# Performance work log

Hardware: AMD Instinct MI355X
Metric: run time of the kernel (lower is better)

The kernel has to match this reference:

```python
import jax, jax.numpy as jnp
import numpy as np
import math

H = 12  # config['n_heads']

def _ln(x, w, b, eps=1e-5):
    mu = x.mean(-1, keepdims=True)
    var = ((x - mu) ** 2).mean(-1, keepdims=True)
    return (x - mu) / jnp.sqrt(var + eps) * w + b

def setup_inputs() -> dict:
    key = jax.random.key(0)
    B, L, D, R = 2, 1024, 768, 128
    d_head = D // H
    ks = jax.random.split(key, 6)
    s = 0.02
    return {
        "x": jax.random.normal(ks[0], (B, L, D), jnp.float32),
        "Wqkv": jax.random.normal(ks[1], (D, 3 * D), jnp.float32) * s,
        "bqkv": jnp.zeros((3 * D,), jnp.float32),
        "Wb1": jax.random.normal(ks[2], (D, R), jnp.float32) * s,
        "Wb2": jax.random.normal(ks[3], (R, H * 5), jnp.float32) * s,
        "temperature": jnp.ones((1,), jnp.float32) * 0.5,
        "Wproj": jax.random.normal(ks[4], (D, D), jnp.float32) * s,
        "bproj": jnp.zeros((D,), jnp.float32),
        "ln_w": jnp.ones((D,), jnp.float32),
        "ln_b": jnp.zeros((D,), jnp.float32),
        "mn_w": jnp.ones((d_head,), jnp.float32),
        "mn_b": jnp.zeros((d_head,), jnp.float32),
    }

def reference(x, Wqkv, bqkv, Wb1, Wb2, temperature, Wproj, bproj, ln_w, ln_b, mn_w, mn_b):
    B, L, D = x.shape
    d = D // H
    x_norm = _ln(x, ln_w, ln_b)
    qkv = x_norm @ Wqkv + bqkv
    q, k, v = jnp.split(qkv, 3, axis=-1)
    # bottleneck gating operates on raw x (not x_norm), matching the source
    params = (jax.nn.silu(x @ Wb1) @ Wb2).reshape(B, L, H, 5)
    sem_amp = jax.nn.sigmoid(params[..., 0])
    sem_phase = jnp.tanh(params[..., 1]) * math.pi
    ctx_amp = jax.nn.sigmoid(params[..., 2])
    ctx_phase = jnp.tanh(params[..., 3]) * math.pi
    # decay_rate = 0.1 + 0.89*sigmoid(params[...,4]) is computed in the source
    # but never used in the final output path, so it is omitted here.
    temp = jnp.clip(temperature, 0.1, 2.0)  # shape (1,), broadcasts
    interference = jnp.tanh(sem_amp * ctx_amp * jnp.cos(sem_phase - ctx_phase)) * temp
    gate = jax.nn.sigmoid(interference)  # [B,L,H]
    q_f = (jax.nn.elu(q) + 1.0).reshape(B, L, H, d)
    k_f = (jax.nn.elu(k) + 1.0).reshape(B, L, H, d)
    v_f = v.reshape(B, L, H, d)
    # gated KV outer products and causal prefix-sum (linear attention state)
    kv_gated = jnp.einsum('blhd,blhe->blhde', k_f, v_f) * (1.0 + gate)[..., None, None]
    kv_states = jnp.cumsum(kv_gated, axis=1)       # [B,L,H,d,d]
    z_states = jnp.cumsum(k_f, axis=1)             # [B,L,H,d]
    out_num = jnp.einsum('blhd,blhde->blhe', q_f, kv_states)
    den = jnp.sum(q_f * z_states, axis=-1, keepdims=True) + 1e-6
    out = _ln(out_num / den, mn_w, mn_b)           # LayerNorm over d_head
    attn_out = out.reshape(B, L, D)
    return (attn_out @ Wproj + bproj, gate)
```

## Files before the change

### kernel.cpp

```cpp
#include <hip/hip_runtime.h>
#include <hip/hip_bf16.h>
#include <math.h>

constexpr int Bc = 2, Lc = 1024, Dc = 768, Hc = 12, dh = 64, Rc = 128;
constexpr int BL = Bc * Lc;
constexpr int TD = 3 * Dc;
constexpr int CH = 64;
constexpr int NC = Lc / CH;
constexpr int BH = Bc * Hc;

typedef __attribute__((ext_vector_type(8))) short bf16x8;
typedef __attribute__((ext_vector_type(4))) float f32x4;

__device__ __forceinline__ float bf2f(short u) {
    union { float f; unsigned int i; } c;
    c.i = ((unsigned int)(unsigned short)u) << 16;
    return c.f;
}
__device__ __forceinline__ short f2b(float f) {
    __hip_bfloat16 h = __float2bfloat16(f);
    return *reinterpret_cast<short*>(&h);
}

#define GLOAD_LDS16(gp, lp)                                                        \
    __builtin_amdgcn_global_load_lds(                                              \
        (const __attribute__((address_space(1))) void*)(gp),                       \
        (__attribute__((address_space(3))) void*)(lp), 16, 0, 0)

__device__ __forceinline__ void do_transpose(const float* __restrict__ W,
                                             __hip_bfloat16* __restrict__ WT,
                                             int K, int N, int bx, int by,
                                             int tid, float* t) {
    int k0 = by * 32, n0 = bx * 32;
    int r = tid >> 5, c = tid & 31;
#pragma unroll
    for (int i = 0; i < 4; i++)
        t[(r + i * 8) * 33 + c] = W[(size_t)(k0 + r + i * 8) * N + n0 + c];
    __syncthreads();
#pragma unroll
    for (int i = 0; i < 4; i++)
        WT[(size_t)(n0 + r + i * 8) * K + k0 + c] = __float2bfloat16(t[c * 33 + r + i * 8]);
}

constexpr int NT1 = (TD / 32) * (Dc / 32);
constexpr int NT2 = (Dc / 32) * (Dc / 32);
constexpr int NT3 = (Rc / 32) * (Dc / 32);
constexpr int NPREP = NT1 + NT2 + NT3 + BL;

__global__ __launch_bounds__(256)
void prep_kernel(const float* __restrict__ x, const float* __restrict__ ln_w,
                 const float* __restrict__ ln_b,
                 const float* __restrict__ Wqkv, const float* __restrict__ Wproj,
                 const float* __restrict__ Wb1,
                 __hip_bfloat16* __restrict__ xnb, __hip_bfloat16* __restrict__ xb,
                 __hip_bfloat16* __restrict__ WqkvT, __hip_bfloat16* __restrict__ WprojT,
                 __hip_bfloat16* __restrict__ Wb1T) {
    __shared__ float shm[32 * 33];
    int bid = blockIdx.x, tid = threadIdx.x;
    if (bid < NT1) { do_transpose(Wqkv, WqkvT, Dc, TD, bid % 72, bid / 72, tid, shm); return; }
    bid -= NT1;
    if (bid < NT2) { do_transpose(Wproj, WprojT, Dc, Dc, bid % 24, bid / 24, tid, shm); return; }
    bid -= NT2;
    if (bid < NT3) { do_transpose(Wb1, Wb1T, Dc, Rc, bid % 4, bid / 4, tid, shm); return; }
    bid -= NT3;
    int row = bid;
    const float* xr = x + (size_t)row * Dc;
    __hip_bfloat16* yr = xnb + (size_t)row * Dc;
    __hip_bfloat16* xbr = xb + (size_t)row * Dc;
    float v[3];
    float s = 0.f;
#pragma unroll
    for (int i = 0; i < 3; i++) { v[i] = xr[tid + i * 256]; s += v[i]; }
    shm[tid] = s; __syncthreads();
    for (int off = 128; off > 0; off >>= 1) {
        if (tid < off) shm[tid] += shm[tid + off];
        __syncthreads();
    }
    float mu = shm[0] / (float)Dc;
    __syncthreads();
    float s2 = 0.f;
#pragma unroll
    for (int i = 0; i < 3; i++) { float d = v[i] - mu; s2 += d * d; }
    shm[tid] = s2; __syncthreads();
    for (int off = 128; off > 0; off >>= 1) {
        if (tid < off) shm[tid] += shm[tid + off];
        __syncthreads();
    }
    float rstd = rsqrtf(shm[0] / (float)Dc + 1e-5f);
#pragma unroll
    for (int i = 0; i < 3; i++) {
        int c = tid + i * 256;
        yr[c] = __float2bfloat16((v[i] - mu) * rstd * ln_w[c] + ln_b[c]);
        xbr[c] = __float2bfloat16(v[i]);
    }
}

constexpr int NQB = (TD / 128) * (BL / 128);
constexpr int NFAT = NQB + BL / 128;
__global__ __launch_bounds__(512)
void fat_gemm_kernel(const __hip_bfloat16* __restrict__ A1,
                     const __hip_bfloat16* __restrict__ B1,
                     const float* __restrict__ bias1,
                     __hip_bfloat16* __restrict__ C1,
                     const __hip_bfloat16* __restrict__ A2,
                     const __hip_bfloat16* __restrict__ B2,
                     float* __restrict__ C2) {
    __shared__ short lds[2][2][128 * 64];
    int bid = blockIdx.x;
    bid = (bid & 7) * (NFAT / 8) + (bid >> 3);
    bool isq = bid < NQB;
    int bx, by, N;
    const __hip_bfloat16 *A, *BT;
    if (isq) { bx = bid % 18; by = bid / 18; A = A1; BT = B1; N = TD; }
    else     { int b2 = bid - NQB; bx = 0; by = b2; A = A2; BT = B2; N = Rc; }
    const int K = Dc;

    int tid = threadIdx.x;
    int wave = tid >> 6, lane = tid & 63;
    int l16 = lane & 15, l4 = lane >> 4;
    int m0 = by * 128, n0 = bx * 128;

    int ab = wave >> 2;
    int r_in = lane >> 3;
    int s_src = (lane & 7) ^ r_in;
    const __hip_bfloat16* gbase = ab ? (BT + (size_t)n0 * K) : (A + (size_t)m0 * K);
    const __hip_bfloat16* gsrc =
        gbase + (size_t)((wave & 3) * 32 + r_in) * K + s_src * 8;

    int wr = (wave >> 2) * 64, wc = (wave & 3) * 32;
    int xs = l16 & 7;

    f32x4 acc[4][2];
#pragma unroll
    for (int i = 0; i < 4; i++)
#pragma unroll
        for (int j = 0; j < 2; j++) acc[i][j] = f32x4{0.f, 0.f, 0.f, 0.f};

    auto stage = [&](int buf, int kt) {
        const __hip_bfloat16* g = gsrc + kt * 64;
        short* lb = &lds[buf][ab][(wave & 3) * 32 * 64];
#pragma unroll
        for (int i = 0; i < 4; i++)
            GLOAD_LDS16(g + (size_t)i * 8 * K, lb + i * 8 * 64);
    };
    auto compute = [&](int buf) {
        const short* As = &lds[buf][0][0];
        const short* Bs = &lds[buf][1][0];
#pragma unroll
        for (int kk = 0; kk < 2; kk++) {
            bf16x8 af[4], bfr[2];
            int slot = (kk * 4 + l4) ^ xs;
#pragma unroll
            for (int f = 0; f < 4; f++)
                af[f] = *reinterpret_cast<const bf16x8*>(
                    &As[(wr + f * 16 + l16) * 64 + slot * 8]);
#pragma unroll
            for (int f = 0; f < 2; f++)
                bfr[f] = *reinterpret_cast<const bf16x8*>(
                    &Bs[(wc + f * 16 + l16) * 64 + slot * 8]);
#pragma unroll
            for (int i = 0; i < 4; i++)
#pragma unroll
                for (int j = 0; j < 2; j++)
                    acc[i][j] = __builtin_amdgcn_mfma_f32_16x16x32_bf16(
                        af[i], bfr[j], acc[i][j], 0, 0, 0);
        }
    };

    int NT = K / 64;
    int cur = 0;
    stage(0, 0);
    __syncthreads();
    for (int t = 0; t < NT; t++) {
        if (t + 1 < NT) stage(cur ^ 1, t + 1);
        compute(cur);
        if (t + 1 < NT) { __syncthreads(); cur ^= 1; }
    }

    int crow = l4 * 4;
#pragma unroll
    for (int i = 0; i < 4; i++) {
#pragma unroll
        for (int j = 0; j < 2; j++) {
            int col = n0 + wc + j * 16 + l16;
            float bb = isq ? bias1[col] : 0.f;
#pragma unroll
            for (int r = 0; r < 4; r++) {
                int rowm = m0 + wr + i * 16 + crow + r;
                float v = acc[i][j][r] + bb;
                if (isq) {
                    C1[(size_t)rowm * N + col] = __float2bfloat16(v);
                } else {
                    v = v / (1.f + expf(-v));
                    C2[(size_t)rowm * N + col] = v;
                }
            }
        }
    }
}

template <bool OUT_BF16, int ACT>
__global__ __launch_bounds__(512)
void gemm_mfma_kernel(const __hip_bfloat16* __restrict__ A,
                      const __hip_bfloat16* __restrict__ BT,
                      const float* __restrict__ bias,
                      void* __restrict__ Cout, int M, int N, int K, int nbx) {
    __shared__ short lds[2][2][128 * 64];
    int nwg = gridDim.x;
    int bid = blockIdx.x;
    if ((nwg & 7) == 0) bid = (bid & 7) * (nwg >> 3) + (bid >> 3);
    int m0 = (bid / nbx) * 128, n0 = (bid % nbx) * 128;

    int tid = threadIdx.x;
    int wave = tid >> 6, lane = tid & 63;
    int l16 = lane & 15, l4 = lane >> 4;

    int ab = wave >> 2;
    int r_in = lane >> 3;
    int s_src = (lane & 7) ^ r_in;
    const __hip_bfloat16* gbase = ab ? (BT + (size_t)n0 * K) : (A + (size_t)m0 * K);
    const __hip_bfloat16* gsrc =
        gbase + (size_t)((wave & 3) * 32 + r_in) * K + s_src * 8;

    int wr = (wave >> 2) * 64, wc = (wave & 3) * 32;
    int xs = l16 & 7;

    f32x4 acc[4][2];
#pragma unroll
    for (int i = 0; i < 4; i++)
#pragma unroll
        for (int j = 0; j < 2; j++) acc[i][j] = f32x4{0.f, 0.f, 0.f, 0.f};

    auto stage = [&](int buf, int kt) {
        const __hip_bfloat16* g = gsrc + kt * 64;
        short* lb = &lds[buf][ab][(wave & 3) * 32 * 64];
#pragma unroll
        for (int i = 0; i < 4; i++)
            GLOAD_LDS16(g + (size_t)i * 8 * K, lb + i * 8 * 64);
    };
    auto compute = [&](int buf) {
        const short* As = &lds[buf][0][0];
        const short* Bs = &lds[buf][1][0];
#pragma unroll
        for (int kk = 0; kk < 2; kk++) {
            bf16x8 af[4], bfr[2];
            int slot = (kk * 4 + l4) ^ xs;
#pragma unroll
            for (int f = 0; f < 4; f++)
                af[f] = *reinterpret_cast<const bf16x8*>(
                    &As[(wr + f * 16 + l16) * 64 + slot * 8]);
#pragma unroll
            for (int f = 0; f < 2; f++)
                bfr[f] = *reinterpret_cast<const bf16x8*>(
                    &Bs[(wc + f * 16 + l16) * 64 + slot * 8]);
#pragma unroll
            for (int i = 0; i < 4; i++)
#pragma unroll
                for (int j = 0; j < 2; j++)
                    acc[i][j] = __builtin_amdgcn_mfma_f32_16x16x32_bf16(
                        af[i], bfr[j], acc[i][j], 0, 0, 0);
        }
    };

    int NT = K / 64;
    int cur = 0;
    stage(0, 0);
    __syncthreads();
    for (int t = 0; t < NT; t++) {
        if (t + 1 < NT) stage(cur ^ 1, t + 1);
        compute(cur);
        if (t + 1 < NT) { __syncthreads(); cur ^= 1; }
    }

    int crow = l4 * 4;
#pragma unroll
    for (int i = 0; i < 4; i++) {
#pragma unroll
        for (int j = 0; j < 2; j++) {
            int col = n0 + wc + j * 16 + l16;
            float bb = bias ? bias[col] : 0.f;
#pragma unroll
            for (int r = 0; r < 4; r++) {
                int rowm = m0 + wr + i * 16 + crow + r;
                float v = acc[i][j][r] + bb;
                if (ACT == 1) v = v / (1.f + expf(-v));
                if (OUT_BF16)
                    ((__hip_bfloat16*)Cout)[(size_t)rowm * N + col] = __float2bfloat16(v);
                else
                    ((float*)Cout)[(size_t)rowm * N + col] = v;
            }
        }
    }
}

__global__ __launch_bounds__(256)
void phaseA_kernel(const __hip_bfloat16* __restrict__ qkv, const float* __restrict__ tbuf,
                   const float* __restrict__ Wb2, const float* __restrict__ temperature,
                   float* __restrict__ gate_out,
                   float* __restrict__ SU, float* __restrict__ zc) {
    int bid = blockIdx.x;
    int bh = bid >> 4, c = bid & 15;
    int b = bh / Hc, h = bh % Hc;
    int tok0 = b * Lc + c * CH;
    __shared__ float Ks[64 * 64];
    __shared__ float Vs[64 * 64];
    __shared__ float ogs[64];
    int tid = threadIdx.x;
#pragma unroll
    for (int i = 0; i < 2; i++) {
        int c8 = tid + i * 256;
        int tt = c8 >> 3, d8 = (c8 & 7) * 8;
        size_t rowoff = (size_t)(tok0 + tt) * TD + h * dh;
        bf16x8 k8 = *reinterpret_cast<const bf16x8*>(qkv + rowoff + Dc + d8);
        bf16x8 v8 = *reinterpret_cast<const bf16x8*>(qkv + rowoff + 2 * Dc + d8);
        float kf[8], vf[8];
#pragma unroll
        for (int j = 0; j < 8; j++) {
            float kv = bf2f(k8[j]);
            kf[j] = kv > 0.f ? kv + 1.f : expf(kv);
            vf[j] = bf2f(v8[j]);
        }
        *reinterpret_cast<float4*>(&Ks[tt * 64 + d8])     = *reinterpret_cast<float4*>(&kf[0]);
        *reinterpret_cast<float4*>(&Ks[tt * 64 + d8 + 4]) = *reinterpret_cast<float4*>(&kf[4]);
        *reinterpret_cast<float4*>(&Vs[tt * 64 + d8])     = *reinterpret_cast<float4*>(&vf[0]);
        *reinterpret_cast<float4*>(&Vs[tt * 64 + d8 + 4]) = *reinterpret_cast<float4*>(&vf[4]);
    }
    if (tid < 64) {
        const float* tr = tbuf + (size_t)(tok0 + tid) * Rc;
        float p0 = 0.f, p1 = 0.f, p2 = 0.f, p3 = 0.f, p4 = 0.f;
#pragma unroll 4
        for (int r = 0; r < Rc; r++) {
            float tv = tr[r];
            const float* wr = Wb2 + r * (Hc * 5) + h * 5;
            p0 = fmaf(tv, wr[0], p0);
            p1 = fmaf(tv, wr[1], p1);
            p2 = fmaf(tv, wr[2], p2);
            p3 = fmaf(tv, wr[3], p3);
            p4 = fmaf(tv, wr[4], p4);
        }
        const float PI = 3.14159265358979323846f;
        float sem_amp = 1.f / (1.f + expf(-p0));
        float sem_phase = tanhf(p1) * PI;
        float ctx_amp = 1.f / (1.f + expf(-p2));
        float ctx_phase = tanhf(p3) * PI;
        float temp = fminf(fmaxf(temperature[0], 0.1f), 2.0f);
        float inter = tanhf(sem_amp * ctx_amp * cosf(sem_phase - ctx_phase)) * temp;
        float g = 1.f / (1.f + expf(-inter));
        gate_out[(size_t)(tok0 + tid) * Hc + h] = g;
        ogs[tid] = 1.f + g;
    }
    __syncthreads();
    int e = tid & 63, d0 = (tid >> 6) * 16;
    float u[16] = {};
    for (int tt = 0; tt < 64; tt++) {
        float vv = Vs[tt * 64 + e] * ogs[tt];
        float4 k4[4];
#pragma unroll
        for (int q = 0; q < 4; q++)
            k4[q] = *reinterpret_cast<const float4*>(&Ks[tt * 64 + d0 + q * 4]);
        const float* kk = reinterpret_cast<const float*>(k4);
#pragma unroll
        for (int j = 0; j < 16; j++)
            u[j] = fmaf(kk[j], vv, u[j]);
    }
    float* Uo = SU + (size_t)bid * 4096 + e * 64 + d0;
#pragma unroll
    for (int q = 0; q < 4; q++)
        *reinterpret_cast<float4*>(Uo + q * 4) =
            make_float4(u[q * 4], u[q * 4 + 1], u[q * 4 + 2], u[q * 4 + 3]);
    if (tid < 64) {
        float zsum = 0.f;
        for (int tt = 0; tt < 64; tt++) zsum += Ks[tt * 64 + tid];
        zc[bid * 64 + tid] = zsum;
    }
}

__global__ __launch_bounds__(256)
void prefix_kernel(float* __restrict__ SU, float* __restrict__ zc) {
    int gid = blockIdx.x * 256 + threadIdx.x;
    if (gid < BH * 4096) {
        int bh = gid >> 12, i = gid & 4095;
        float* S = SU + (size_t)bh * NC * 4096 + i;
        float r[NC];
#pragma unroll
        for (int cc = 0; cc < NC; cc++) r[cc] = S[cc * 4096];
        float run = 0.f;
#pragma unroll
        for (int cc = 0; cc < NC; cc++) { float tv = r[cc]; S[cc * 4096] = run; run += tv; }
    } else {
        int g2 = gid - BH * 4096;
        if (g2 < BH * 64) {
            int bh = g2 >> 6, i = g2 & 63;
            float* z = zc + (size_t)bh * NC * 64 + i;
            float r[NC];
#pragma unroll
            for (int cc = 0; cc < NC; cc++) r[cc] = z[cc * 64];
            float run = 0.f;
#pragma unroll
            for (int cc = 0; cc < NC; cc++) { float tv = r[cc]; z[cc * 64] = run; run += tv; }
        }
    }
}

constexpr int LQ = 72;
constexpr int LB = 136;
__global__ __launch_bounds__(256)
void phaseC_kernel(const __hip_bfloat16* __restrict__ qkv, const float* __restrict__ gate,
                   const float* __restrict__ SU, const float* __restrict__ zc,
                   const float* __restrict__ mn_w, const float* __restrict__ mn_b,
                   __hip_bfloat16* __restrict__ attn) {
    int bid = blockIdx.x;
    int bh = bid >> 4;
    int b = bh / Hc, h = bh % Hc;
    int tok0 = b * Lc + (bid & 15) * CH;
    __shared__ short Qs[64 * LQ];
    __shared__ short Ks[64 * LQ];
    __shared__ short Ps[64 * LQ];
    __shared__ short Bst[80 * LB];
    int tid = threadIdx.x;
    int wave = tid >> 6, lane = tid & 63;
    int l16 = lane & 15, l4 = lane >> 4;

    const float* SUp = SU + (size_t)bid * 4096;
    const float* zcp = zc + (size_t)bid * 64;

#pragma unroll
    for (int i = 0; i < 2; i++) {
        int c8 = tid + i * 256;
        int tt = c8 >> 3, d8 = (c8 & 7) * 8;
        size_t rowoff = (size_t)(tok0 + tt) * TD + h * dh;
        bf16x8 q8 = *reinterpret_cast<const bf16x8*>(qkv + rowoff + d8);
        bf16x8 k8 = *reinterpret_cast<const bf16x8*>(qkv + rowoff + Dc + d8);
        bf16x8 v8 = *reinterpret_cast<const bf16x8*>(qkv + rowoff + 2 * Dc + d8);
        float gv = 1.f + gate[(size_t)(tok0 + tt) * Hc + h];
        short qo[8], ko[8];
#pragma unroll
        for (int j = 0; j < 8; j++) {
            float qv = bf2f(q8[j]);
            qo[j] = f2b(qv > 0.f ? qv + 1.f : expf(qv));
            float kv = bf2f(k8[j]);
            ko[j] = f2b(kv > 0.f ? kv + 1.f : expf(kv));
            Bst[(d8 + j) * LB + tt] = f2b(bf2f(v8[j]) * gv);
        }
        *reinterpret_cast<bf16x8*>(&Qs[tt * LQ + d8]) = *reinterpret_cast<bf16x8*>(qo);
        *reinterpret_cast<bf16x8*>(&Ks[tt * LQ + d8]) = *reinterpret_cast<bf16x8*>(ko);
        float4 sa = *reinterpret_cast<const float4*>(SUp + tt * 64 + d8);
        float4 sb = *reinterpret_cast<const float4*>(SUp + tt * 64 + d8 + 4);
        short so[8] = { f2b(sa.x), f2b(sa.y), f2b(sa.z), f2b(sa.w),
                        f2b(sb.x), f2b(sb.y), f2b(sb.z), f2b(sb.w) };
        *reinterpret_cast<bf16x8*>(&Bst[tt * LB + 64 + d8]) = *reinterpret_cast<bf16x8*>(so);
    }
    if (tid < 64) {
        Bst[64 * LB + tid] = f2b(1.0f);
        Bst[64 * LB + 64 + tid] = f2b(zcp[tid]);
    } else {
        for (int i2 = tid - 64; i2 < 15 * LB; i2 += 192) Bst[65 * LB + i2] = 0;
    }
    __syncthreads();

    const short* arow = &Qs[(wave * 16 + l16) * LQ];
    f32x4 accp[4];
#pragma unroll
    for (int j = 0; j < 4; j++) accp[j] = f32x4{0.f, 0.f, 0.f, 0.f};
#pragma unroll
    for (int kk = 0; kk < 2; kk++) {
        bf16x8 af = *reinterpret_cast<const bf16x8*>(&arow[kk * 32 + l4 * 8]);
#pragma unroll
        for (int j = 0; j < 4; j++) {
            bf16x8 bfv = *reinterpret_cast<const bf16x8*>(
                &Ks[(j * 16 + l16) * LQ + kk * 32 + l4 * 8]);
            accp[j] = __builtin_amdgcn_mfma_f32_16x16x32_bf16(af, bfv, accp[j], 0, 0, 0);
        }
    }
#pragma unroll
    for (int j = 0; j < 4; j++) {
#pragma unroll
        for (int r = 0; r < 4; r++) {
            int l = wave * 16 + l4 * 4 + r;
            int t = j * 16 + l16;
            float pv = (t <= l) ? accp[j][r] : 0.f;
            Ps[l * LQ + t] = f2b(pv);
        }
    }
    __syncthreads();

    const short* prow = &Ps[(wave * 16 + l16) * LQ];
    f32x4 acc[5];
#pragma unroll
    for (int j = 0; j < 5; j++) acc[j] = f32x4{0.f, 0.f, 0.f, 0.f};
#pragma unroll
    for (int kk = 0; kk < 4; kk++) {
        bf16x8 af = (kk < 2)
            ? *reinterpret_cast<const bf16x8*>(&prow[kk * 32 + l4 * 8])
            : *reinterpret_cast<const bf16x8*>(&arow[(kk - 2) * 32 + l4 * 8]);
#pragma unroll
        for (int j = 0; j < 5; j++) {
            bf16x8 bfv = *reinterpret_cast<const bf16x8*>(
                &Bst[(j * 16 + l16) * LB + kk * 32 + l4 * 8]);
            acc[j] = __builtin_amdgcn_mfma_f32_16x16x32_bf16(af, bfv, acc[j], 0, 0, 0);
        }
    }

#pragma unroll
    for (int r = 0; r < 4; r++) {
        float den = __shfl(acc[4][r], l4 * 16) + 1e-6f;
        float inv = 1.f / den;
        float v0 = acc[0][r] * inv, v1 = acc[1][r] * inv;
        float v2 = acc[2][r] * inv, v3 = acc[3][r] * inv;
        float s1 = v0 + v1 + v2 + v3;
        float s2 = v0 * v0 + v1 * v1 + v2 * v2 + v3 * v3;
#pragma unroll
        for (int m = 1; m < 16; m <<= 1) {
            s1 += __shfl_xor(s1, m, 64);
            s2 += __shfl_xor(s2, m, 64);
        }
        float mu = s1 * (1.f / 64.f);
        float rstd = rsqrtf(s2 * (1.f / 64.f) - mu * mu + 1e-5f);
        int l = wave * 16 + l4 * 4 + r;
        __hip_bfloat16* orow = attn + (size_t)(tok0 + l) * Dc + h * dh;
        float vj[4] = {v0, v1, v2, v3};
#pragma unroll
        for (int j = 0; j < 4; j++) {
            int e = j * 16 + l16;
            orow[e] = __float2bfloat16((vj[j] - mu) * rstd * mn_w[e] + mn_b[e]);
        }
    }
}

extern "C" void kernel_launch(void* const* d_in, const int* in_sizes, int n_in,
                              void* d_out, int out_size, void* d_ws, size_t ws_size,
                              hipStream_t stream) {
    const float* x     = (const float*)d_in[0];
    const float* Wqkv  = (const float*)d_in[1];
    const float* bqkv  = (const float*)d_in[2];
    const float* Wb1   = (const float*)d_in[3];
    const float* Wb2   = (const float*)d_in[4];
    const float* temp  = (const float*)d_in[5];
    const float* Wproj = (const float*)d_in[6];
    const float* bproj = (const float*)d_in[7];
    const float* ln_w  = (const float*)d_in[8];
    const float* ln_b  = (const float*)d_in[9];
    const float* mn_w  = (const float*)d_in[10];
    const float* mn_b  = (const float*)d_in[11];

    float* out0 = (float*)d_out;
    float* gate = out0 + (size_t)BL * Dc;

    float* ws   = (float*)d_ws;
    float* tbuf = ws;
    float* SU   = tbuf + (size_t)BL * Rc;
    float* zc   = SU + (size_t)BH * NC * 4096;
    __hip_bfloat16* bfr = (__hip_bfloat16*)(zc + (size_t)BH * NC * 64);
    __hip_bfloat16* qkvb   = bfr;
    __hip_bfloat16* xnb    = qkvb + (size_t)BL * TD;
    __hip_bfloat16* xb     = xnb + (size_t)BL * Dc;
    __hip_bfloat16* attnb  = xb + (size_t)BL * Dc;
    __hip_bfloat16* WqkvT  = attnb + (size_t)BL * Dc;
    __hip_bfloat16* WprojT = WqkvT + (size_t)TD * Dc;
    __hip_bfloat16* Wb1T   = WprojT + (size_t)Dc * Dc;

    prep_kernel<<<NPREP, 256, 0, stream>>>(x, ln_w, ln_b, Wqkv, Wproj, Wb1,
                                           xnb, xb, WqkvT, WprojT, Wb1T);
    fat_gemm_kernel<<<NFAT, 512, 0, stream>>>(xnb, WqkvT, bqkv, qkvb, xb, Wb1T, tbuf);
    phaseA_kernel<<<BH * NC, 256, 0, stream>>>(qkvb, tbuf, Wb2, temp, gate, SU, zc);
    prefix_kernel<<<(BH * 4096 + BH * 64 + 255) / 256, 256, 0, stream>>>(SU, zc);
    phaseC_kernel<<<BH * NC, 256, 0, stream>>>(qkvb, gate, SU, zc, mn_w, mn_b, attnb);
    gemm_mfma_kernel<false, 0><<<(Dc / 128) * (BL / 128), 512, 0, stream>>>(
        attnb, WprojT, bproj, out0, BL, Dc, Dc, Dc / 128);
}
```

Baseline: 69.94 us.

## Use MFMA for chunk KV state in phaseA and shrink projection GEMM tiles

The per-chunk K^T·(gated V) outer-product sum in phaseA moves from scalar FMAs to bf16 MFMA. K and gated V are stored transposed in LDS, and a ones-row appended to V yields the z column sums from the same MMA. The gate bottleneck dot product is spread over 4 threads per token, with Wb2 staged in LDS and a shuffle reduction. The output projection GEMM switches from 128x128 tiles with 512 threads to 64x64 tiles with 256 threads, giving 384 blocks instead of 96 to fill more CUs. The risk is bf16 rounding of the gated V and K values in the state computation.

```diff
diff --git a/kernel.cpp b/kernel.cpp
--- a/kernel.cpp
+++ b/kernel.cpp
@@ -199,62 +199,59 @@
     }
 }
 
-template <bool OUT_BF16, int ACT>
-__global__ __launch_bounds__(512)
-void gemm_mfma_kernel(const __hip_bfloat16* __restrict__ A,
-                      const __hip_bfloat16* __restrict__ BT,
-                      const float* __restrict__ bias,
-                      void* __restrict__ Cout, int M, int N, int K, int nbx) {
-    __shared__ short lds[2][2][128 * 64];
+__global__ __launch_bounds__(256)
+void gemm64_kernel(const __hip_bfloat16* __restrict__ A,
+                   const __hip_bfloat16* __restrict__ BT,
+                   const float* __restrict__ bias,
+                   float* __restrict__ C, int M, int N, int K, int nbx) {
+    __shared__ short lds[2][128 * 64];
     int nwg = gridDim.x;
     int bid = blockIdx.x;
     if ((nwg & 7) == 0) bid = (bid & 7) * (nwg >> 3) + (bid >> 3);
-    int m0 = (bid / nbx) * 128, n0 = (bid % nbx) * 128;
+    int m0 = (bid / nbx) * 64, n0 = (bid % nbx) * 64;
 
     int tid = threadIdx.x;
     int wave = tid >> 6, lane = tid & 63;
     int l16 = lane & 15, l4 = lane >> 4;
 
-    int ab = wave >> 2;
     int r_in = lane >> 3;
     int s_src = (lane & 7) ^ r_in;
-    const __hip_bfloat16* gbase = ab ? (BT + (size_t)n0 * K) : (A + (size_t)m0 * K);
-    const __hip_bfloat16* gsrc =
-        gbase + (size_t)((wave & 3) * 32 + r_in) * K + s_src * 8;
-
-    int wr = (wave >> 2) * 64, wc = (wave & 3) * 32;
+    const __hip_bfloat16* gsrc = (wave < 2)
+        ? A  + (size_t)(m0 + wave * 32 + r_in) * K + s_src * 8
+        : BT + (size_t)(n0 + (wave - 2) * 32 + r_in) * K + s_src * 8;
+
+    int wr = (wave >> 1) * 32, wc = (wave & 1) * 32;
     int xs = l16 & 7;
 
-    f32x4 acc[4][2];
-#pragma unroll
-    for (int i = 0; i < 4; i++)
+    f32x4 acc[2][2];
+#pragma unroll
+    for (int i = 0; i < 2; i++)
 #pragma unroll
         for (int j = 0; j < 2; j++) acc[i][j] = f32x4{0.f, 0.f, 0.f, 0.f};
 
     auto stage = [&](int buf, int kt) {
         const __hip_bfloat16* g = gsrc + kt * 64;
-        short* lb = &lds[buf][ab][(wave & 3) * 32 * 64];
+        short* lb = &lds[buf][wave * 32 * 64];
 #pragma unroll
         for (int i = 0; i < 4; i++)
             GLOAD_LDS16(g + (size_t)i * 8 * K, lb + i * 8 * 64);
     };
     auto compute = [&](int buf) {
-        const short* As = &lds[buf][0][0];
-        const short* Bs = &lds[buf][1][0];
+        const short* As = &lds[buf][0];
+        const short* Bs = &lds[buf][64 * 64];
 #pragma unroll
         for (int kk = 0; kk < 2; kk++) {
-            bf16x8 af[4], bfr[2];
+            bf16x8 af[2], bfr[2];
             int slot = (kk * 4 + l4) ^ xs;
 #pragma unroll
-            for (int f = 0; f < 4; f++)
-                af[f] = *reinterpret_cast<const bf16x8*>(
+            for (int f = 0; f < 2; f++) {
+                af[f]  = *reinterpret_cast<const bf16x8*>(
                     &As[(wr + f * 16 + l16) * 64 + slot * 8]);
-#pragma unroll
-            for (int f = 0; f < 2; f++)
                 bfr[f] = *reinterpret_cast<const bf16x8*>(
                     &Bs[(wc + f * 16 + l16) * 64 + slot * 8]);
-#pragma unroll
-            for (int i = 0; i < 4; i++)
+            }
+#pragma unroll
+            for (int i = 0; i < 2; i++)
 #pragma unroll
                 for (int j = 0; j < 2; j++)
                     acc[i][j] = __builtin_amdgcn_mfma_f32_16x16x32_bf16(
@@ -274,25 +271,21 @@
 
     int crow = l4 * 4;
 #pragma unroll
-    for (int i = 0; i < 4; i++) {
+    for (int i = 0; i < 2; i++) {
 #pragma unroll
         for (int j = 0; j < 2; j++) {
             int col = n0 + wc + j * 16 + l16;
-            float bb = bias ? bias[col] : 0.f;
+            float bb = bias[col];
 #pragma unroll
             for (int r = 0; r < 4; r++) {
                 int rowm = m0 + wr + i * 16 + crow + r;
-                float v = acc[i][j][r] + bb;
-                if (ACT == 1) v = v / (1.f + expf(-v));
-                if (OUT_BF16)
-                    ((__hip_bfloat16*)Cout)[(size_t)rowm * N + col] = __float2bfloat16(v);
-                else
-                    ((float*)Cout)[(size_t)rowm * N + col] = v;
+                C[(size_t)rowm * N + col] = acc[i][j][r] + bb;
             }
         }
     }
 }
 
+constexpr int LQ = 72;
 __global__ __launch_bounds__(256)
 void phaseA_kernel(const __hip_bfloat16* __restrict__ qkv, const float* __restrict__ tbuf,
                    const float* __restrict__ Wb2, const float* __restrict__ temperature,
@@ -302,76 +295,105 @@
     int bh = bid >> 4, c = bid & 15;
     int b = bh / Hc, h = bh % Hc;
     int tok0 = b * Lc + c * CH;
-    __shared__ float Ks[64 * 64];
-    __shared__ float Vs[64 * 64];
+    __shared__ short KsT[64 * LQ];
+    __shared__ short VT[80 * LQ];
+    __shared__ float w2s[5 * 128];
     __shared__ float ogs[64];
     int tid = threadIdx.x;
+    int wave = tid >> 6, lane = tid & 63;
+    int l16 = lane & 15, l4 = lane >> 4;
+
+    for (int i = tid; i < 640; i += 256) {
+        int cc = i >> 7, r = i & 127;
+        w2s[i] = Wb2[r * (Hc * 5) + h * 5 + cc];
+    }
+    bf16x8 k8[2], v8[2];
 #pragma unroll
     for (int i = 0; i < 2; i++) {
         int c8 = tid + i * 256;
         int tt = c8 >> 3, d8 = (c8 & 7) * 8;
         size_t rowoff = (size_t)(tok0 + tt) * TD + h * dh;
-        bf16x8 k8 = *reinterpret_cast<const bf16x8*>(qkv + rowoff + Dc + d8);
-        bf16x8 v8 = *reinterpret_cast<const bf16x8*>(qkv + rowoff + 2 * Dc + d8);
-        float kf[8], vf[8];
+        k8[i] = *reinterpret_cast<const bf16x8*>(qkv + rowoff + Dc + d8);
+        v8[i] = *reinterpret_cast<const bf16x8*>(qkv + rowoff + 2 * Dc + d8);
+    }
+    for (int i = tid; i < 16 * LQ; i += 256) VT[64 * LQ + i] = 0;
+    if (tid < 64) VT[64 * LQ + tid] = f2b(1.0f);
+    __syncthreads();
+
+    {
+        int tt = tid >> 2, sub = tid & 3;
+        const float* tr = tbuf + (size_t)(tok0 + tt) * Rc + sub * 32;
+        float p[5] = {};
+        for (int r4 = 0; r4 < 32; r4 += 4) {
+            float4 tv = *reinterpret_cast<const float4*>(tr + r4);
+#pragma unroll
+            for (int cc = 0; cc < 5; cc++) {
+                float4 w4 = *reinterpret_cast<const float4*>(&w2s[cc * 128 + sub * 32 + r4]);
+                p[cc] = fmaf(tv.x, w4.x, fmaf(tv.y, w4.y,
+                        fmaf(tv.z, w4.z, fmaf(tv.w, w4.w, p[cc]))));
+            }
+        }
+#pragma unroll
+        for (int cc = 0; cc < 5; cc++) {
+            p[cc] += __shfl_xor(p[cc], 1, 64);
+            p[cc] += __shfl_xor(p[cc], 2, 64);
+        }
+        if (sub == 0) {
+            const float PI = 3.14159265358979323846f;
+            float sem_amp = 1.f / (1.f + expf(-p[0]));
+            float sem_phase = tanhf(p[1]) * PI;
+            float ctx_amp = 1.f / (1.f + expf(-p[2]));
+            float ctx_phase = tanhf(p[3]) * PI;
+            float temp = fminf(fmaxf(temperature[0], 0.1f), 2.0f);
+            float inter = tanhf(sem_amp * ctx_amp * cosf(sem_phase - ctx_phase)) * temp;
+            float g = 1.f / (1.f + expf(-inter));
+            gate_out[(size_t)(tok0 + tt) * Hc + h] = g;
+            ogs[tt] = 1.f + g;
+        }
+    }
+    __syncthreads();
+
+#pragma unroll
+    for (int i = 0; i < 2; i++) {
+        int c8 = tid + i * 256;
+        int tt = c8 >> 3, d8 = (c8 & 7) * 8;
+        float gv = ogs[tt];
 #pragma unroll
         for (int j = 0; j < 8; j++) {
-            float kv = bf2f(k8[j]);
-            kf[j] = kv > 0.f ? kv + 1.f : expf(kv);
-            vf[j] = bf2f(v8[j]);
-        }
-        *reinterpret_cast<float4*>(&Ks[tt * 64 + d8])     = *reinterpret_cast<float4*>(&kf[0]);
-        *reinterpret_cast<float4*>(&Ks[tt * 64 + d8 + 4]) = *reinterpret_cast<float4*>(&kf[4]);
-        *reinterpret_cast<float4*>(&Vs[tt * 64 + d8])     = *reinterpret_cast<float4*>(&vf[0]);
-        *reinterpret_cast<float4*>(&Vs[tt * 64 + d8 + 4]) = *reinterpret_cast<float4*>(&vf[4]);
-    }
-    if (tid < 64) {
-        const float* tr = tbuf + (size_t)(tok0 + tid) * Rc;
-        float p0 = 0.f, p1 = 0.f, p2 = 0.f, p3 = 0.f, p4 = 0.f;
-#pragma unroll 4
-        for (int r = 0; r < Rc; r++) {
-            float tv = tr[r];
-            const float* wr = Wb2 + r * (Hc * 5) + h * 5;
-            p0 = fmaf(tv, wr[0], p0);
-            p1 = fmaf(tv, wr[1], p1);
-            p2 = fmaf(tv, wr[2], p2);
-            p3 = fmaf(tv, wr[3], p3);
-            p4 = fmaf(tv, wr[4], p4);
-        }
-        const float PI = 3.14159265358979323846f;
-        float sem_amp = 1.f / (1.f + expf(-p0));
-        float sem_phase = tanhf(p1) * PI;
-        float ctx_amp = 1.f / (1.f + expf(-p2));
-        float ctx_phase = tanhf(p3) * PI;
-        float temp = fminf(fmaxf(temperature[0], 0.1f), 2.0f);
-        float inter = tanhf(sem_amp * ctx_amp * cosf(sem_phase - ctx_phase)) * temp;
-        float g = 1.f / (1.f + expf(-inter));
-        gate_out[(size_t)(tok0 + tid) * Hc + h] = g;
-        ogs[tid] = 1.f + g;
-    }
-    __syncthreads();
-    int e = tid & 63, d0 = (tid >> 6) * 16;
-    float u[16] = {};
-    for (int tt = 0; tt < 64; tt++) {
-        float vv = Vs[tt * 64 + e] * ogs[tt];
-        float4 k4[4];
-#pragma unroll
-        for (int q = 0; q < 4; q++)
-            k4[q] = *reinterpret_cast<const float4*>(&Ks[tt * 64 + d0 + q * 4]);
-        const float* kk = reinterpret_cast<const float*>(k4);
-#pragma unroll
-        for (int j = 0; j < 16; j++)
-            u[j] = fmaf(kk[j], vv, u[j]);
-    }
-    float* Uo = SU + (size_t)bid * 4096 + e * 64 + d0;
-#pragma unroll
-    for (int q = 0; q < 4; q++)
-        *reinterpret_cast<float4*>(Uo + q * 4) =
-            make_float4(u[q * 4], u[q * 4 + 1], u[q * 4 + 2], u[q * 4 + 3]);
-    if (tid < 64) {
-        float zsum = 0.f;
-        for (int tt = 0; tt < 64; tt++) zsum += Ks[tt * 64 + tid];
-        zc[bid * 64 + tid] = zsum;
+            float kv = bf2f(k8[i][j]);
+            KsT[(d8 + j) * LQ + tt] = f2b(kv > 0.f ? kv + 1.f : expf(kv));
+            VT[(d8 + j) * LQ + tt]  = f2b(bf2f(v8[i][j]) * gv);
+        }
+    }
+    __syncthreads();
+
+    const short* arow = &KsT[(wave * 16 + l16) * LQ];
+    f32x4 acc[5];
+#pragma unroll
+    for (int j = 0; j < 5; j++) acc[j] = f32x4{0.f, 0.f, 0.f, 0.f};
+#pragma unroll
+    for (int kk = 0; kk < 2; kk++) {
+        bf16x8 af = *reinterpret_cast<const bf16x8*>(&arow[kk * 32 + l4 * 8]);
+#pragma unroll
+        for (int j = 0; j < 5; j++) {
+            bf16x8 bfv = *reinterpret_cast<const bf16x8*>(
+                &VT[(j * 16 + l16) * LQ + kk * 32 + l4 * 8]);
+            acc[j] = __builtin_amdgcn_mfma_f32_16x16x32_bf16(af, bfv, acc[j], 0, 0, 0);
+        }
+    }
+    int dbase = wave * 16 + l4 * 4;
+    float* SUo = SU + (size_t)bid * 4096;
+#pragma unroll
+    for (int j = 0; j < 4; j++) {
+        int e = j * 16 + l16;
+#pragma unroll
+        for (int r = 0; r < 4; r++)
+            SUo[e * 64 + dbase + r] = acc[j][r];
+    }
+    if (l16 == 0) {
+#pragma unroll
+        for (int r = 0; r < 4; r++)
+            zc[bid * 64 + dbase + r] = acc[4][r];
     }
 }
 
@@ -402,7 +424,6 @@
     }
 }
 
-constexpr int LQ = 72;
 constexpr int LB = 136;
 __global__ __launch_bounds__(256)
 void phaseC_kernel(const __hip_bfloat16* __restrict__ qkv, const float* __restrict__ gate,
@@ -565,6 +586,6 @@
     phaseA_kernel<<<BH * NC, 256, 0, stream>>>(qkvb, tbuf, Wb2, temp, gate, SU, zc);
     prefix_kernel<<<(BH * 4096 + BH * 64 + 255) / 256, 256, 0, stream>>>(SU, zc);
     phaseC_kernel<<<BH * NC, 256, 0, stream>>>(qkvb, gate, SU, zc, mn_w, mn_b, attnb);
-    gemm_mfma_kernel<false, 0><<<(Dc / 128) * (BL / 128), 512, 0, stream>>>(
-        attnb, WprojT, bproj, out0, BL, Dc, Dc, Dc / 128);
-}
+    gemm64_kernel<<<(BL / 64) * (Dc / 64), 256, 0, stream>>>(
+        attnb, WprojT, bproj, out0, BL, Dc, Dc, Dc / 64);
+}
```

Result: faster. 58.21 us, median of 2 (-16.8%).
